# Kernel tuning notes

Hardware: AMD Instinct MI355X
Metric: run time of the kernel (lower is better)

## Reference

```python
import jax, jax.numpy as jnp
import numpy as np

B, S, H = 1, 4096, 2048
NH, HD = 16, 128  # num_heads, head_dim = H // NH


def setup_inputs() -> dict:
    key = jax.random.key(0)
    k1, k2, k3 = jax.random.split(key, 3)
    x = jax.random.normal(k1, (B, S, H), dtype=jnp.float32)
    w_qkv = jax.random.normal(k2, (3 * H, H), dtype=jnp.float32) * (1.0 / np.sqrt(H))
    w_out = jax.random.normal(k3, (H, H), dtype=jnp.float32) * (1.0 / np.sqrt(H))
    return {"x": x, "w_qkv": w_qkv, "w_out": w_out}


def reference(x, w_qkv, w_out):
    b, s, _ = x.shape
    # qkv projection: torch Linear computes x @ W^T
    qkv = jnp.einsum('bsh,oh->bso', x, w_qkv)
    qkv = qkv.reshape(b, s, 3, NH, HD).transpose(2, 0, 3, 1, 4)  # [3,B,NH,S,HD]
    q, k, v = qkv[0], qkv[1], qkv[2]
    # world_size == 1 -> single ring step == full attention with online softmax
    scores = jnp.einsum('bhqd,bhkd->bhqk', q, k) / np.sqrt(HD)
    m = jnp.max(scores, axis=-1, keepdims=True)          # running max (single step)
    p = jnp.exp(scores - m)                              # scores_exp
    out = jnp.einsum('bhqk,bhkd->bhqd', p, v)
    denom = jnp.sum(p, axis=-1, keepdims=True) + 1e-8    # running_sum + eps
    out = out / denom
    out = out.transpose(0, 2, 1, 3).reshape(b, s, H)     # [B,S,H]
    return jnp.einsum('bsh,oh->bso', out, w_out)
```

## Files before the change

kernel.cpp:

```cpp
#include <hip/hip_runtime.h>
#include <stdint.h>

typedef __attribute__((ext_vector_type(4))) float f32x4;
typedef __attribute__((ext_vector_type(16))) float f32x16;
typedef __attribute__((ext_vector_type(8))) short bf16x8;
typedef unsigned short u16;

#define MFMA(a, b, c) __builtin_amdgcn_mfma_f32_16x16x32_bf16(a, b, c, 0, 0, 0)
#define MFMA32(a, b, c) __builtin_amdgcn_mfma_f32_32x32x16_bf16(a, b, c, 0, 0, 0)
#define EXP2(x) __builtin_amdgcn_exp2f(x)
#define FENCE asm volatile("" ::: "memory")
#define BARRIER do { FENCE; __builtin_amdgcn_s_barrier(); FENCE; } while (0)

__device__ __forceinline__ u16 f2bf(float f) {
  union { float f; unsigned u; } x; x.f = f;
  unsigned r = x.u + 0x7fffu + ((x.u >> 16) & 1u);
  return (u16)(r >> 16);
}

__device__ __forceinline__ unsigned cvtpk(float lo, float hi) {
  unsigned r;
  asm("v_cvt_pk_bf16_f32 %0, %1, %2" : "=v"(r) : "v"(lo), "v"(hi));
  return r;
}

__device__ __forceinline__ void pl32swap(unsigned& a, unsigned& b) {
  asm volatile("v_permlane32_swap_b32 %0, %1" : "+v"(a), "+v"(b));
}

__device__ __forceinline__ void gload16(const void* g, void* l) {
  __builtin_amdgcn_global_load_lds(
      (const __attribute__((address_space(1))) unsigned int*)g,
      (__attribute__((address_space(3))) unsigned int*)l, 16, 0, 0);
}

__global__ void __launch_bounds__(256) cast_bf16(const float* __restrict__ in,
                                                 u16* __restrict__ out, int n4) {
  int i = blockIdx.x * 256 + threadIdx.x;
  if (i >= n4) return;
  float4 v = reinterpret_cast<const float4*>(in)[i];
  ushort4 o;
  o.x = f2bf(v.x); o.y = f2bf(v.y); o.z = f2bf(v.z); o.w = f2bf(v.w);
  reinterpret_cast<ushort4*>(out)[i] = o;
}

template <int EPI>
__global__ void __launch_bounds__(512)
gemm8(const u16* __restrict__ A, const u16* __restrict__ B,
      void* __restrict__ C0, void* __restrict__ C1, void* __restrict__ C2,
      int M, int N, int K, int MBt) {
  __shared__ alignas(16) char smb[131072];
  const int tid = threadIdx.x;
  const int w = tid >> 6, lane = tid & 63;
  const int lr = lane & 15, g = lane >> 4;
  const int wm = w >> 2, wn = w & 3;
  const int gb = (blockIdx.x & 7) * ((int)gridDim.x >> 3) + (blockIdx.x >> 3);
  const int mb = gb % MBt, nb = gb / MBt;
  const int m0 = mb * 256, n0 = nb * 256;
  const int NT = K >> 6, NIT = NT >> 1;

  const int l8 = lane >> 3, l7 = lane & 7;
  const int csb = (l7 ^ l8) * 16;
  const char* asrcb[2];
  const char* bsrcb[2];
  unsigned adst[2], bdst[2];
#pragma unroll
  for (int j = 0; j < 2; ++j) {
    int c = 2 * w + j;
    int ra = (c & 7) * 8 + ((c >> 3) << 7) + l8;
    asrcb[j] = (const char*)(A + (size_t)(m0 + ra) * K) + csb;
    adst[j] = (unsigned)(ra * 128 + l7 * 16);
    int rb = (c & 3) * 8 + ((c >> 2) << 6) + l8;
    bsrcb[j] = (const char*)(B + (size_t)(n0 + rb) * K) + csb;
    bdst[j] = (unsigned)(rb * 128 + l7 * 16);
  }
  const size_t arow64 = (size_t)64 * K * 2;
  const size_t brow32 = (size_t)32 * K * 2;

#define STG(kt, u)                                                            \
  do {                                                                        \
    if ((kt) < NT) {                                                          \
      int _d = ((kt) & 1) ? 32768 : 0;                                        \
      size_t _ko = (size_t)(kt) * 128;                                        \
      if ((u) == 0) {                                                         \
        gload16(asrcb[0] + _ko, smb + _d + adst[0]);                          \
        gload16(asrcb[1] + _ko, smb + _d + adst[1]);                          \
      } else if ((u) == 1) {                                                  \
        gload16(bsrcb[0] + _ko, smb + 65536 + _d + bdst[0]);                  \
        gload16(bsrcb[1] + _ko, smb + 65536 + _d + bdst[1]);                  \
      } else if ((u) == 2) {                                                  \
        gload16(asrcb[0] + arow64 + _ko, smb + _d + 8192 + adst[0]);          \
        gload16(asrcb[1] + arow64 + _ko, smb + _d + 8192 + adst[1]);          \
      } else {                                                                \
        gload16(bsrcb[0] + brow32 + _ko, smb + 65536 + _d + 4096 + bdst[0]);  \
        gload16(bsrcb[1] + brow32 + _ko, smb + 65536 + _d + 4096 + bdst[1]);  \
      }                                                                       \
    }                                                                         \
  } while (0)

  f32x4 acc[8][4];
#pragma unroll
  for (int x = 0; x < 8; ++x)
#pragma unroll
    for (int y = 0; y < 4; ++y) acc[x][y] = f32x4{0.f, 0.f, 0.f, 0.f};
  bf16x8 af[4][2], bf01[2][2], bf23[2][2];
  const int aoff0 = ((g) ^ (lr & 7)) << 4;
  const int aoff1 = ((4 + g) ^ (lr & 7)) << 4;
  const int arow = (wm * 128 + lr) * 128;
  const int brow = (wn * 64 + lr) * 128;

  auto LDA = [&](const char* base, int mih) {
#pragma unroll
    for (int mi = 0; mi < 4; ++mi) {
      const char* p = base + arow + (mih * 64 + mi * 16) * 128;
      af[mi][0] = *(const bf16x8*)(p + aoff0);
      af[mi][1] = *(const bf16x8*)(p + aoff1);
    }
  };
  auto LDB = [&](const char* base, bf16x8 (*bfr)[2], int nih) {
#pragma unroll
    for (int ni = 0; ni < 2; ++ni) {
      const char* p = base + brow + (nih * 32 + ni * 16) * 128;
      bfr[ni][0] = *(const bf16x8*)(p + aoff0);
      bfr[ni][1] = *(const bf16x8*)(p + aoff1);
    }
  };
  auto MM = [&](int mih, int nih, bf16x8 (*bfr)[2]) {
    __builtin_amdgcn_s_setprio(1);
#pragma unroll
    for (int mi = 0; mi < 4; ++mi)
#pragma unroll
      for (int ni = 0; ni < 2; ++ni) {
        acc[mih * 4 + mi][nih * 2 + ni] =
            MFMA(af[mi][0], bfr[ni][0], acc[mih * 4 + mi][nih * 2 + ni]);
        acc[mih * 4 + mi][nih * 2 + ni] =
            MFMA(af[mi][1], bfr[ni][1], acc[mih * 4 + mi][nih * 2 + ni]);
      }
    __builtin_amdgcn_s_setprio(0);
  };

  STG(0, 0); STG(0, 1); STG(0, 2); STG(0, 3);
  STG(1, 0); STG(1, 1); STG(1, 2);
  asm volatile("s_waitcnt vmcnt(6)" ::: "memory");
  BARRIER;

  const char* A0 = smb;
  const char* B0 = smb + 65536;
  const char* A1 = smb + 32768;
  const char* B1 = smb + 65536 + 32768;

  for (int it = 0; it < NIT; ++it) {
    const int t0 = 2 * it;
    const bool lastit = (it == NIT - 1);
    LDA(A0, 0); LDB(B0, bf01, 0); STG(t0 + 1, 3);
    BARRIER; MM(0, 0, bf01); BARRIER;
    LDB(B0, bf23, 1); STG(t0 + 2, 0);
    BARRIER; MM(0, 1, bf23); BARRIER;
    LDA(A0, 1); STG(t0 + 2, 1);
    BARRIER; MM(1, 1, bf23); BARRIER;
    STG(t0 + 2, 2);
    if (lastit) asm volatile("s_waitcnt vmcnt(0)" ::: "memory");
    else        asm volatile("s_waitcnt vmcnt(6)" ::: "memory");
    BARRIER; MM(1, 0, bf01); BARRIER;
    LDA(A1, 0); LDB(B1, bf01, 0); STG(t0 + 2, 3);
    BARRIER; MM(0, 0, bf01); BARRIER;
    LDB(B1, bf23, 1); STG(t0 + 3, 0);
    BARRIER; MM(0, 1, bf23); BARRIER;
    LDA(A1, 1); STG(t0 + 3, 1);
    BARRIER; MM(1, 1, bf23); BARRIER;
    STG(t0 + 3, 2);
    asm volatile("s_waitcnt vmcnt(6)" ::: "memory");
    BARRIER; MM(1, 0, bf01); BARRIER;
  }
#undef STG

  if (EPI == 0) {
    const float qs = 0.08838834764831845f * 1.4426950408889634f;
    u16* qo = (u16*)C0;
    u16* ko = (u16*)C1;
    u16* vo = (u16*)C2;
#pragma unroll
    for (int mi = 0; mi < 8; ++mi) {
      int s0 = m0 + wm * 128 + mi * 16 + g * 4;
#pragma unroll
      for (int ni = 0; ni < 4; ++ni) {
        int n = n0 + wn * 64 + ni * 16 + lr;
        int t = n >> 11, hh = (n >> 7) & 15, d = n & 127;
        if (t == 2) {
          ushort4 pk;
          pk.x = f2bf(acc[mi][ni][0]);
          pk.y = f2bf(acc[mi][ni][1]);
          pk.z = f2bf(acc[mi][ni][2]);
          pk.w = f2bf(acc[mi][ni][3]);
          *(ushort4*)(vo + (size_t)(hh * 128 + d) * 4096 + s0) = pk;
        } else {
          float sc = (t == 0) ? qs : 1.f;
          u16* dq = (t == 0 ? qo : ko) + (size_t)(hh * 4096 + s0) * 128 + d;
#pragma unroll
          for (int j = 0; j < 4; ++j) dq[(size_t)j * 128] = f2bf(acc[mi][ni][j] * sc);
        }
      }
    }
  } else {
    float* C = (float*)C0;
#pragma unroll
    for (int mi = 0; mi < 8; ++mi)
#pragma unroll
      for (int ni = 0; ni < 4; ++ni) {
        size_t r0 = (size_t)(m0 + wm * 128 + mi * 16 + g * 4);
        int cn = n0 + wn * 64 + ni * 16 + lr;
#pragma unroll
        for (int j = 0; j < 4; ++j) C[(r0 + j) * N + cn] = acc[mi][ni][j];
      }
  }
}

template <int EPI>
__global__ void __launch_bounds__(256, 2)
gemm_bt(const u16* __restrict__ A, const u16* __restrict__ B,
        void* __restrict__ C0, void* __restrict__ C1, void* __restrict__ C2,
        int M, int N, int K, int MB) {
  __shared__ alignas(16) u16 sm[8192];
  const int tid = threadIdx.x;
  const int w = tid >> 6, lane = tid & 63;
  const int lr = lane & 15, g = lane >> 4;
  const int gb = (blockIdx.x & 7) * ((int)gridDim.x >> 3) + (blockIdx.x >> 3);
  const int mb = gb % MB, nb = gb / MB;
  const int m0 = mb * 128, n0 = nb * 128;

  const u16* src[4];
  u16* dst[4];
#pragma unroll
  for (int i = 0; i < 4; ++i) {
    int c = w * 4 + i;
    int r = (c & 7) * 16 + (lane >> 2);
    int sb = (lane & 3) ^ ((r >> 1) & 3);
    src[i] = (c < 8) ? (A + (size_t)(m0 + r) * K + sb * 8)
                     : (B + (size_t)(n0 + r) * K + sb * 8);
    dst[i] = &sm[c * 512];
  }

  f32x4 acc[4][4];
#pragma unroll
  for (int x = 0; x < 4; ++x)
#pragma unroll
    for (int y = 0; y < 4; ++y) acc[x][y] = f32x4{0.f, 0.f, 0.f, 0.f};

  const int rowb = (w >> 1) * 64, colb = (w & 1) * 64;
  const int nk = K >> 5;
  for (int kt = 0; kt < nk; ++kt) {
#pragma unroll
    for (int i = 0; i < 4; ++i) gload16(src[i] + kt * 32, dst[i]);
    __syncthreads();
    bf16x8 af[4], bfr[4];
#pragma unroll
    for (int mi = 0; mi < 4; ++mi) {
      int r = rowb + mi * 16 + lr;
      af[mi] = *(const bf16x8*)((const char*)sm + r * 64 +
                                ((g * 16) ^ (((r >> 1) & 3) << 4)));
    }
#pragma unroll
    for (int ni = 0; ni < 4; ++ni) {
      int r = colb + ni * 16 + lr;
      bfr[ni] = *(const bf16x8*)((const char*)sm + 8192 + r * 64 +
                                 ((g * 16) ^ (((r >> 1) & 3) << 4)));
    }
#pragma unroll
    for (int mi = 0; mi < 4; ++mi)
#pragma unroll
      for (int ni = 0; ni < 4; ++ni)
        acc[mi][ni] = MFMA(af[mi], bfr[ni], acc[mi][ni]);
    __syncthreads();
  }

  float* C = (float*)C0;
#pragma unroll
  for (int mi = 0; mi < 4; ++mi)
#pragma unroll
    for (int ni = 0; ni < 4; ++ni) {
      size_t r0 = (size_t)(m0 + rowb + mi * 16 + g * 4);
      int cn = n0 + colb + ni * 16 + lr;
#pragma unroll
      for (int j = 0; j < 4; ++j) C[(r0 + j) * N + cn] = acc[mi][ni][j];
    }
}

__global__ void __launch_bounds__(512)
attn_kernel(const u16* __restrict__ qg, const u16* __restrict__ kg,
            const u16* __restrict__ vtg, u16* __restrict__ og) {
  __shared__ alignas(16) u16 sm[32768];
  const int tid = threadIdx.x;
  const int w = tid >> 6, lane = tid & 63;
  const int ql = lane & 31, hl = lane >> 5;
  const int gb = (blockIdx.x & 7) * 32 + (blockIdx.x >> 3);
  const int h = gb >> 4;
  const int qb = gb & 15;

  const u16* ssrc[4];
  u16* sdst[4];
  size_t sstep;
  if (w < 4) {
    sstep = 64 * 128;
#pragma unroll
    for (int i = 0; i < 4; ++i) {
      int c = w * 4 + i;
      int r = c * 4 + (lane >> 4);
      int sb = (lane & 15) ^ (r & 15);
      ssrc[i] = kg + (size_t)(h * 4096 + r) * 128 + sb * 8;
      sdst[i] = &sm[c * 512];
    }
  } else {
    sstep = 64;
#pragma unroll
    for (int i = 0; i < 4; ++i) {
      int c = (w - 4) * 4 + i;
      int j = c * 4 + (lane >> 4);
      int x = (lane & 15) ^ (j & 15);
      int e = x >> 3, b = x & 7;
      ssrc[i] = vtg + (size_t)(h * 128 + 2 * j + e) * 4096 + b * 8;
      sdst[i] = &sm[16384 + c * 512];
    }
  }

  const u16* qrow = qg + (size_t)(h * 4096 + qb * 256 + w * 32 + ql) * 128 + hl * 8;
  bf16x8 qf[8];
#pragma unroll
  for (int s = 0; s < 8; ++s) qf[s] = *(const bf16x8*)(qrow + s * 16);

  f32x16 of[4];
#pragma unroll
  for (int i = 0; i < 4; ++i)
#pragma unroll
    for (int r = 0; r < 16; ++r) of[i][r] = 0.f;
  float mrun = -1e30f, lsum = 0.f;
  const float thr = 6.0f;

#pragma unroll
  for (int i = 0; i < 4; ++i) gload16(ssrc[i], sdst[i]);

  const int kxor = (ql & 15) << 4;
  const int ve8 = (ql & 1) << 3, vxor = ql >> 1;
  for (int t = 0; t < 64; ++t) {
    const int cur = t & 1;
    asm volatile("s_waitcnt vmcnt(0)" ::: "memory");
    __builtin_amdgcn_s_barrier();
    FENCE;
    if (t + 1 < 64) {
      const int nb = (t + 1) & 1;
#pragma unroll
      for (int i = 0; i < 4; ++i)
        gload16(ssrc[i] + (size_t)(t + 1) * sstep, sdst[i] + nb * 8192);
    }
    const char* kbuf = (const char*)sm + cur * 16384;
    const char* vbuf = (const char*)sm + 32768 + cur * 16384;

    f32x16 st0, st1;
#pragma unroll
    for (int r = 0; r < 16; ++r) { st0[r] = 0.f; st1[r] = 0.f; }
    __builtin_amdgcn_s_setprio(1);
#pragma unroll
    for (int s = 0; s < 8; ++s) {
      int off = ((s * 2 + hl) << 4) ^ kxor;
      bf16x8 k0 = *(const bf16x8*)(kbuf + ql * 256 + off);
      bf16x8 k1 = *(const bf16x8*)(kbuf + (32 + ql) * 256 + off);
      st0 = MFMA32(k0, qf[s], st0);
      st1 = MFMA32(k1, qf[s], st1);
    }
    __builtin_amdgcn_s_setprio(0);

    float tmax = -1e30f;
#pragma unroll
    for (int r = 0; r < 16; ++r) tmax = fmaxf(tmax, fmaxf(st0[r], st1[r]));
    tmax = fmaxf(tmax, __shfl_xor(tmax, 32));
    if (!__all(tmax - mrun <= thr)) {
      float mnew = fmaxf(mrun, tmax);
      float esc = EXP2(mrun - mnew);
#pragma unroll
      for (int db = 0; db < 4; ++db)
#pragma unroll
        for (int r = 0; r < 16; ++r) of[db][r] *= esc;
      lsum *= esc;
      mrun = mnew;
    }
    float psum = 0.f;
    unsigned pk0[8], pk1[8];
#pragma unroll
    for (int i = 0; i < 8; ++i) {
      float a0 = EXP2(st0[2 * i] - mrun);
      float b0 = EXP2(st0[2 * i + 1] - mrun);
      float a1 = EXP2(st1[2 * i] - mrun);
      float b1 = EXP2(st1[2 * i + 1] - mrun);
      psum += (a0 + b0) + (a1 + b1);
      pk0[i] = cvtpk(a0, b0);
      pk1[i] = cvtpk(a1, b1);
    }
    psum += __shfl_xor(psum, 32);
    lsum += psum;

    pl32swap(pk0[0], pk0[2]); pl32swap(pk0[1], pk0[3]);
    pl32swap(pk0[4], pk0[6]); pl32swap(pk0[5], pk0[7]);
    pl32swap(pk1[0], pk1[2]); pl32swap(pk1[1], pk1[3]);
    pl32swap(pk1[4], pk1[6]); pl32swap(pk1[5], pk1[7]);
    union U { unsigned u[4]; bf16x8 v; };
    U paf[4];
#pragma unroll
    for (int i = 0; i < 4; ++i) { paf[0].u[i] = pk0[i]; paf[1].u[i] = pk0[4 + i]; }
#pragma unroll
    for (int i = 0; i < 4; ++i) { paf[2].u[i] = pk1[i]; paf[3].u[i] = pk1[4 + i]; }

    __builtin_amdgcn_s_setprio(1);
#pragma unroll
    for (int db = 0; db < 4; ++db) {
      const char* vrow = vbuf + (db * 16 + vxor) * 256;
#pragma unroll
      for (int kp = 0; kp < 4; ++kp) {
        int m = (ve8 | (kp * 2 + hl)) ^ vxor;
        bf16x8 vf = *(const bf16x8*)(vrow + m * 16);
        of[db] = MFMA32(vf, paf[kp].v, of[db]);
      }
    }
    __builtin_amdgcn_s_setprio(0);
    FENCE;
  }

  float linv = 1.f / (lsum + 1e-8f);
  size_t qrow_o = (size_t)(qb * 256 + w * 32 + ql) * 2048 + h * 128;
#pragma unroll
  for (int db = 0; db < 4; ++db)
#pragma unroll
    for (int u = 0; u < 4; ++u) {
      ushort4 pk;
      pk.x = f2bf(of[db][4 * u + 0] * linv);
      pk.y = f2bf(of[db][4 * u + 1] * linv);
      pk.z = f2bf(of[db][4 * u + 2] * linv);
      pk.w = f2bf(of[db][4 * u + 3] * linv);
      *(ushort4*)(og + qrow_o + db * 32 + 8 * u + hl * 4) = pk;
    }
}

extern "C" void kernel_launch(void* const* d_in, const int* in_sizes, int n_in,
                              void* d_out, int out_size, void* d_ws, size_t ws_size,
                              hipStream_t stream) {
  const float* x = (const float*)d_in[0];
  const float* w_qkv = (const float*)d_in[1];
  const float* w_out = (const float*)d_in[2];

  char* ws = (char*)d_ws;
  u16* xb = (u16*)(ws + 0);
  u16* wqkvb = (u16*)(ws + 16777216);
  u16* woutb = (u16*)(ws + 41943040);
  u16* qb = (u16*)(ws + 50331648);
  u16* kb = (u16*)(ws + 67108864);
  u16* vtb = (u16*)(ws + 83886080);
  u16* aob = (u16*)(ws + 100663296);

  cast_bf16<<<8192, 256, 0, stream>>>(x, xb, 2097152);
  cast_bf16<<<12288, 256, 0, stream>>>(w_qkv, wqkvb, 3145728);
  cast_bf16<<<4096, 256, 0, stream>>>(w_out, woutb, 1048576);

  gemm8<0><<<384, 512, 0, stream>>>(xb, wqkvb, qb, kb, vtb, 4096, 6144, 2048, 16);
  attn_kernel<<<256, 512, 0, stream>>>(qb, kb, vtb, aob);
  gemm_bt<1><<<32 * 16, 256, 0, stream>>>(aob, woutb, d_out, nullptr, nullptr, 4096, 2048, 2048, 32);
}
```

Before: 339.6 us.

## Split attention KV range across two wave groups with LDS merge of partials

The attention kernel now handles 128 query rows per block instead of 256, doubling the grid to 512 blocks. Each block's two groups of four waves process separate halves of the key/value sequence (split-K), each with its own smaller 32-key double-buffered tiles. At the end the two partial softmax states (max, sum, output accumulators) are exchanged through LDS and merged by the first group before writing. The aim is more blocks across the 256 CUs and less work per wave per tile. The cost is an extra LDS round trip, a merge step, and a larger LDS footprint (about 66 KB), which may limit blocks per CU.

```diff
diff --git a/kernel.cpp b/kernel.cpp
--- a/kernel.cpp
+++ b/kernel.cpp
@@ -288,41 +288,46 @@
 __global__ void __launch_bounds__(512)
 attn_kernel(const u16* __restrict__ qg, const u16* __restrict__ kg,
             const u16* __restrict__ vtg, u16* __restrict__ og) {
-  __shared__ alignas(16) u16 sm[32768];
+  __shared__ alignas(64) char smb[67584];
   const int tid = threadIdx.x;
   const int w = tid >> 6, lane = tid & 63;
   const int ql = lane & 31, hl = lane >> 5;
-  const int gb = (blockIdx.x & 7) * 32 + (blockIdx.x >> 3);
-  const int h = gb >> 4;
-  const int qb = gb & 15;
+  const int gb = (blockIdx.x & 7) * 64 + (blockIdx.x >> 3);
+  const int h = gb >> 5;
+  const int qb = gb & 31;
+  const int g2 = w >> 2;
+  const int qw = w & 3;
 
   const u16* ssrc[4];
-  u16* sdst[4];
+  unsigned sdst[4];
   size_t sstep;
-  if (w < 4) {
-    sstep = 64 * 128;
-#pragma unroll
-    for (int i = 0; i < 4; ++i) {
-      int c = w * 4 + i;
-      int r = c * 4 + (lane >> 4);
-      int sb = (lane & 15) ^ (r & 15);
-      ssrc[i] = kg + (size_t)(h * 4096 + r) * 128 + sb * 8;
-      sdst[i] = &sm[c * 512];
-    }
-  } else {
-    sstep = 64;
-#pragma unroll
-    for (int i = 0; i < 4; ++i) {
-      int c = (w - 4) * 4 + i;
-      int j = c * 4 + (lane >> 4);
-      int x = (lane & 15) ^ (j & 15);
-      int e = x >> 3, b = x & 7;
-      ssrc[i] = vtg + (size_t)(h * 128 + 2 * j + e) * 4096 + b * 8;
-      sdst[i] = &sm[16384 + c * 512];
-    }
-  }
-
-  const u16* qrow = qg + (size_t)(h * 4096 + qb * 256 + w * 32 + ql) * 128 + hl * 8;
+  {
+    const int sg = w >> 2;
+    if (!((w >> 1) & 1)) {
+      sstep = 32 * 128;
+#pragma unroll
+      for (int i = 0; i < 4; ++i) {
+        int c = (w & 1) * 4 + i;
+        int r = c * 4 + (lane >> 4);
+        int sb = (lane & 15) ^ (r & 15);
+        ssrc[i] = kg + (size_t)(h * 4096 + sg * 2048 + r) * 128 + sb * 8;
+        sdst[i] = sg * 16384 + c * 1024;
+      }
+    } else {
+      sstep = 32;
+#pragma unroll
+      for (int i = 0; i < 4; ++i) {
+        int c = (w & 1) * 4 + i;
+        int j = c * 4 + (lane >> 4);
+        int x = (lane & 15) ^ (j & 15);
+        int e = x >> 2, b = x & 3;
+        ssrc[i] = vtg + (size_t)(h * 128 + 4 * j + e) * 4096 + sg * 2048 + b * 8;
+        sdst[i] = 32768 + sg * 16384 + c * 1024;
+      }
+    }
+  }
+
+  const u16* qrow = qg + (size_t)(h * 4096 + qb * 128 + qw * 32 + ql) * 128 + hl * 8;
   bf16x8 qf[8];
 #pragma unroll
   for (int s = 0; s < 8; ++s) qf[s] = *(const bf16x8*)(qrow + s * 16);
@@ -336,10 +341,14 @@
   const float thr = 6.0f;
 
 #pragma unroll
-  for (int i = 0; i < 4; ++i) gload16(ssrc[i], sdst[i]);
+  for (int i = 0; i < 4; ++i) gload16(ssrc[i], smb + sdst[i]);
 
   const int kxor = (ql & 15) << 4;
-  const int ve8 = (ql & 1) << 3, vxor = ql >> 1;
+  const char* kbase = smb + g2 * 16384;
+  const char* vbase = smb + 32768 + g2 * 16384;
+  const int vj = ql >> 2;
+  const int vm0 = (ql & 3) << 2;
+
   for (int t = 0; t < 64; ++t) {
     const int cur = t & 1;
     asm volatile("s_waitcnt vmcnt(0)" ::: "memory");
@@ -349,28 +358,26 @@
       const int nb = (t + 1) & 1;
 #pragma unroll
       for (int i = 0; i < 4; ++i)
-        gload16(ssrc[i] + (size_t)(t + 1) * sstep, sdst[i] + nb * 8192);
-    }
-    const char* kbuf = (const char*)sm + cur * 16384;
-    const char* vbuf = (const char*)sm + 32768 + cur * 16384;
-
-    f32x16 st0, st1;
-#pragma unroll
-    for (int r = 0; r < 16; ++r) { st0[r] = 0.f; st1[r] = 0.f; }
+        gload16(ssrc[i] + (size_t)(t + 1) * sstep, smb + sdst[i] + nb * 8192);
+    }
+    const char* kbuf = kbase + cur * 8192;
+    const char* vbuf = vbase + cur * 8192;
+
+    f32x16 st0;
+#pragma unroll
+    for (int r = 0; r < 16; ++r) st0[r] = 0.f;
     __builtin_amdgcn_s_setprio(1);
 #pragma unroll
     for (int s = 0; s < 8; ++s) {
       int off = ((s * 2 + hl) << 4) ^ kxor;
       bf16x8 k0 = *(const bf16x8*)(kbuf + ql * 256 + off);
-      bf16x8 k1 = *(const bf16x8*)(kbuf + (32 + ql) * 256 + off);
       st0 = MFMA32(k0, qf[s], st0);
-      st1 = MFMA32(k1, qf[s], st1);
     }
     __builtin_amdgcn_s_setprio(0);
 
     float tmax = -1e30f;
 #pragma unroll
-    for (int r = 0; r < 16; ++r) tmax = fmaxf(tmax, fmaxf(st0[r], st1[r]));
+    for (int r = 0; r < 16; ++r) tmax = fmaxf(tmax, st0[r]);
     tmax = fmaxf(tmax, __shfl_xor(tmax, 32));
     if (!__all(tmax - mrun <= thr)) {
       float mnew = fmaxf(mrun, tmax);
@@ -383,38 +390,32 @@
       mrun = mnew;
     }
     float psum = 0.f;
-    unsigned pk0[8], pk1[8];
+    unsigned pk0[8];
 #pragma unroll
     for (int i = 0; i < 8; ++i) {
       float a0 = EXP2(st0[2 * i] - mrun);
       float b0 = EXP2(st0[2 * i + 1] - mrun);
-      float a1 = EXP2(st1[2 * i] - mrun);
-      float b1 = EXP2(st1[2 * i + 1] - mrun);
-      psum += (a0 + b0) + (a1 + b1);
+      psum += a0 + b0;
       pk0[i] = cvtpk(a0, b0);
-      pk1[i] = cvtpk(a1, b1);
     }
     psum += __shfl_xor(psum, 32);
     lsum += psum;
 
     pl32swap(pk0[0], pk0[2]); pl32swap(pk0[1], pk0[3]);
     pl32swap(pk0[4], pk0[6]); pl32swap(pk0[5], pk0[7]);
-    pl32swap(pk1[0], pk1[2]); pl32swap(pk1[1], pk1[3]);
-    pl32swap(pk1[4], pk1[6]); pl32swap(pk1[5], pk1[7]);
     union U { unsigned u[4]; bf16x8 v; };
-    U paf[4];
+    U paf[2];
 #pragma unroll
     for (int i = 0; i < 4; ++i) { paf[0].u[i] = pk0[i]; paf[1].u[i] = pk0[4 + i]; }
-#pragma unroll
-    for (int i = 0; i < 4; ++i) { paf[2].u[i] = pk1[i]; paf[3].u[i] = pk1[4 + i]; }
 
     __builtin_amdgcn_s_setprio(1);
 #pragma unroll
     for (int db = 0; db < 4; ++db) {
-      const char* vrow = vbuf + (db * 16 + vxor) * 256;
-#pragma unroll
-      for (int kp = 0; kp < 4; ++kp) {
-        int m = (ve8 | (kp * 2 + hl)) ^ vxor;
+      int j = db * 8 + vj;
+      const char* vrow = vbuf + j * 256;
+#pragma unroll
+      for (int kp = 0; kp < 2; ++kp) {
+        int m = (vm0 | (kp * 2 + hl)) ^ (j & 15);
         bf16x8 vf = *(const bf16x8*)(vrow + m * 16);
         of[db] = MFMA32(vf, paf[kp].v, of[db]);
       }
@@ -423,19 +424,40 @@
     FENCE;
   }
 
-  float linv = 1.f / (lsum + 1e-8f);
-  size_t qrow_o = (size_t)(qb * 256 + w * 32 + ql) * 2048 + h * 128;
-#pragma unroll
-  for (int db = 0; db < 4; ++db)
-#pragma unroll
-    for (int u = 0; u < 4; ++u) {
-      ushort4 pk;
-      pk.x = f2bf(of[db][4 * u + 0] * linv);
-      pk.y = f2bf(of[db][4 * u + 1] * linv);
-      pk.z = f2bf(of[db][4 * u + 2] * linv);
-      pk.w = f2bf(of[db][4 * u + 3] * linv);
-      *(ushort4*)(og + qrow_o + db * 32 + 8 * u + hl * 4) = pk;
-    }
+  __syncthreads();
+  if (w >= 4) {
+    char* base = smb + qw * 16384 + lane * 256;
+#pragma unroll
+    for (int db = 0; db < 4; ++db) *(f32x16*)(base + db * 64) = of[db];
+    float2 ml;
+    ml.x = mrun; ml.y = lsum;
+    *(float2*)(smb + 65536 + (qw * 64 + lane) * 8) = ml;
+  }
+  __syncthreads();
+  if (w < 4) {
+    const char* base = smb + qw * 16384 + lane * 256;
+    float2 ml = *(const float2*)(smb + 65536 + (qw * 64 + lane) * 8);
+    float m = fmaxf(mrun, ml.x);
+    float a0 = EXP2(mrun - m);
+    float a1 = EXP2(ml.x - m);
+    float l = lsum * a0 + ml.y * a1;
+    float linv = 1.f / (l + 1e-8f);
+    float fa0 = a0 * linv, fa1 = a1 * linv;
+    size_t qrow_o = (size_t)(qb * 128 + qw * 32 + ql) * 2048 + h * 128;
+#pragma unroll
+    for (int db = 0; db < 4; ++db) {
+      f32x16 ob = *(const f32x16*)(base + db * 64);
+#pragma unroll
+      for (int u = 0; u < 4; ++u) {
+        ushort4 pk;
+        pk.x = f2bf(of[db][4 * u + 0] * fa0 + ob[4 * u + 0] * fa1);
+        pk.y = f2bf(of[db][4 * u + 1] * fa0 + ob[4 * u + 1] * fa1);
+        pk.z = f2bf(of[db][4 * u + 2] * fa0 + ob[4 * u + 2] * fa1);
+        pk.w = f2bf(of[db][4 * u + 3] * fa0 + ob[4 * u + 3] * fa1);
+        *(ushort4*)(og + qrow_o + db * 32 + 8 * u + hl * 4) = pk;
+      }
+    }
+  }
 }
 
 extern "C" void kernel_launch(void* const* d_in, const int* in_sizes, int n_in,
@@ -459,6 +481,6 @@
   cast_bf16<<<4096, 256, 0, stream>>>(w_out, woutb, 1048576);
 
   gemm8<0><<<384, 512, 0, stream>>>(xb, wqkvb, qb, kb, vtb, 4096, 6144, 2048, 16);
-  attn_kernel<<<256, 512, 0, stream>>>(qb, kb, vtb, aob);
+  attn_kernel<<<512, 512, 0, stream>>>(qb, kb, vtb, aob);
   gemm_bt<1><<<32 * 16, 256, 0, stream>>>(aob, woutb, d_out, nullptr, nullptr, 4096, 2048, 2048, 32);
 }
```

Result: slower. 362.1 us (+6.6%).

## Widen attention KV tile to 128 keys and reuse gemm8 for output projection

Applied to the files above, without the earlier changes.

The attention kernel now processes 128 keys per iteration instead of 64. That halves the loop trip count and the barrier count, using 128KB of double-buffered LDS with a simpler swizzled V layout. The output projection switches from the small 128x128 gemm_bt kernel to the larger-tile gemm8 kernel in its fp32 epilogue mode, and gemm_bt is deleted. The trade-offs are more registers for four score accumulators, a full 128KB of LDS per attention block, and only 128 blocks for the final GEMM, which may underfill the 256 CUs.

```diff
diff --git a/kernel.cpp b/kernel.cpp
--- a/kernel.cpp
+++ b/kernel.cpp
@@ -215,80 +215,10 @@
   }
 }
 
-template <int EPI>
-__global__ void __launch_bounds__(256, 2)
-gemm_bt(const u16* __restrict__ A, const u16* __restrict__ B,
-        void* __restrict__ C0, void* __restrict__ C1, void* __restrict__ C2,
-        int M, int N, int K, int MB) {
-  __shared__ alignas(16) u16 sm[8192];
-  const int tid = threadIdx.x;
-  const int w = tid >> 6, lane = tid & 63;
-  const int lr = lane & 15, g = lane >> 4;
-  const int gb = (blockIdx.x & 7) * ((int)gridDim.x >> 3) + (blockIdx.x >> 3);
-  const int mb = gb % MB, nb = gb / MB;
-  const int m0 = mb * 128, n0 = nb * 128;
-
-  const u16* src[4];
-  u16* dst[4];
-#pragma unroll
-  for (int i = 0; i < 4; ++i) {
-    int c = w * 4 + i;
-    int r = (c & 7) * 16 + (lane >> 2);
-    int sb = (lane & 3) ^ ((r >> 1) & 3);
-    src[i] = (c < 8) ? (A + (size_t)(m0 + r) * K + sb * 8)
-                     : (B + (size_t)(n0 + r) * K + sb * 8);
-    dst[i] = &sm[c * 512];
-  }
-
-  f32x4 acc[4][4];
-#pragma unroll
-  for (int x = 0; x < 4; ++x)
-#pragma unroll
-    for (int y = 0; y < 4; ++y) acc[x][y] = f32x4{0.f, 0.f, 0.f, 0.f};
-
-  const int rowb = (w >> 1) * 64, colb = (w & 1) * 64;
-  const int nk = K >> 5;
-  for (int kt = 0; kt < nk; ++kt) {
-#pragma unroll
-    for (int i = 0; i < 4; ++i) gload16(src[i] + kt * 32, dst[i]);
-    __syncthreads();
-    bf16x8 af[4], bfr[4];
-#pragma unroll
-    for (int mi = 0; mi < 4; ++mi) {
-      int r = rowb + mi * 16 + lr;
-      af[mi] = *(const bf16x8*)((const char*)sm + r * 64 +
-                                ((g * 16) ^ (((r >> 1) & 3) << 4)));
-    }
-#pragma unroll
-    for (int ni = 0; ni < 4; ++ni) {
-      int r = colb + ni * 16 + lr;
-      bfr[ni] = *(const bf16x8*)((const char*)sm + 8192 + r * 64 +
-                                 ((g * 16) ^ (((r >> 1) & 3) << 4)));
-    }
-#pragma unroll
-    for (int mi = 0; mi < 4; ++mi)
-#pragma unroll
-      for (int ni = 0; ni < 4; ++ni)
-        acc[mi][ni] = MFMA(af[mi], bfr[ni], acc[mi][ni]);
-    __syncthreads();
-  }
-
-  float* C = (float*)C0;
-#pragma unroll
-  for (int mi = 0; mi < 4; ++mi)
-#pragma unroll
-    for (int ni = 0; ni < 4; ++ni) {
-      size_t r0 = (size_t)(m0 + rowb + mi * 16 + g * 4);
-      int cn = n0 + colb + ni * 16 + lr;
-#pragma unroll
-      for (int j = 0; j < 4; ++j) C[(r0 + j) * N + cn] = acc[mi][ni][j];
-    }
-}
-
 __global__ void __launch_bounds__(512)
 attn_kernel(const u16* __restrict__ qg, const u16* __restrict__ kg,
             const u16* __restrict__ vtg, u16* __restrict__ og) {
-  __shared__ alignas(16) u16 sm[32768];
+  __shared__ alignas(64) char smb[131072];
   const int tid = threadIdx.x;
   const int w = tid >> 6, lane = tid & 63;
   const int ql = lane & 31, hl = lane >> 5;
@@ -296,29 +226,28 @@
   const int h = gb >> 4;
   const int qb = gb & 15;
 
-  const u16* ssrc[4];
-  u16* sdst[4];
+  const u16* ssrc[8];
+  unsigned sdst[8];
   size_t sstep;
   if (w < 4) {
-    sstep = 64 * 128;
-#pragma unroll
-    for (int i = 0; i < 4; ++i) {
-      int c = w * 4 + i;
+    sstep = 128 * 128;
+#pragma unroll
+    for (int i = 0; i < 8; ++i) {
+      int c = w * 8 + i;
       int r = c * 4 + (lane >> 4);
       int sb = (lane & 15) ^ (r & 15);
       ssrc[i] = kg + (size_t)(h * 4096 + r) * 128 + sb * 8;
-      sdst[i] = &sm[c * 512];
+      sdst[i] = c * 1024;
     }
   } else {
-    sstep = 64;
-#pragma unroll
-    for (int i = 0; i < 4; ++i) {
-      int c = (w - 4) * 4 + i;
-      int j = c * 4 + (lane >> 4);
-      int x = (lane & 15) ^ (j & 15);
-      int e = x >> 3, b = x & 7;
-      ssrc[i] = vtg + (size_t)(h * 128 + 2 * j + e) * 4096 + b * 8;
-      sdst[i] = &sm[16384 + c * 512];
+    sstep = 128;
+#pragma unroll
+    for (int i = 0; i < 8; ++i) {
+      int c = (w - 4) * 8 + i;
+      int r = c * 4 + (lane >> 4);
+      int sb = (lane & 15) ^ (r & 15);
+      ssrc[i] = vtg + (size_t)(h * 128 + r) * 4096 + sb * 8;
+      sdst[i] = 65536 + c * 1024;
     }
   }
 
@@ -336,41 +265,48 @@
   const float thr = 6.0f;
 
 #pragma unroll
-  for (int i = 0; i < 4; ++i) gload16(ssrc[i], sdst[i]);
+  for (int i = 0; i < 8; ++i) gload16(ssrc[i], smb + sdst[i]);
 
   const int kxor = (ql & 15) << 4;
-  const int ve8 = (ql & 1) << 3, vxor = ql >> 1;
-  for (int t = 0; t < 64; ++t) {
+  for (int t = 0; t < 32; ++t) {
     const int cur = t & 1;
     asm volatile("s_waitcnt vmcnt(0)" ::: "memory");
     __builtin_amdgcn_s_barrier();
     FENCE;
-    if (t + 1 < 64) {
+    if (t + 1 < 32) {
       const int nb = (t + 1) & 1;
 #pragma unroll
-      for (int i = 0; i < 4; ++i)
-        gload16(ssrc[i] + (size_t)(t + 1) * sstep, sdst[i] + nb * 8192);
-    }
-    const char* kbuf = (const char*)sm + cur * 16384;
-    const char* vbuf = (const char*)sm + 32768 + cur * 16384;
-
-    f32x16 st0, st1;
-#pragma unroll
-    for (int r = 0; r < 16; ++r) { st0[r] = 0.f; st1[r] = 0.f; }
+      for (int i = 0; i < 8; ++i)
+        gload16(ssrc[i] + (size_t)(t + 1) * sstep, smb + sdst[i] + nb * 32768);
+    }
+    const char* kbuf = smb + cur * 32768;
+    const char* vbuf = smb + 65536 + cur * 32768;
+
+    f32x16 st[4];
+#pragma unroll
+    for (int kb = 0; kb < 4; ++kb)
+#pragma unroll
+      for (int r = 0; r < 16; ++r) st[kb][r] = 0.f;
     __builtin_amdgcn_s_setprio(1);
 #pragma unroll
     for (int s = 0; s < 8; ++s) {
       int off = ((s * 2 + hl) << 4) ^ kxor;
-      bf16x8 k0 = *(const bf16x8*)(kbuf + ql * 256 + off);
-      bf16x8 k1 = *(const bf16x8*)(kbuf + (32 + ql) * 256 + off);
-      st0 = MFMA32(k0, qf[s], st0);
-      st1 = MFMA32(k1, qf[s], st1);
+      bf16x8 k0 = *(const bf16x8*)(kbuf + (0 * 32 + ql) * 256 + off);
+      bf16x8 k1 = *(const bf16x8*)(kbuf + (1 * 32 + ql) * 256 + off);
+      bf16x8 k2 = *(const bf16x8*)(kbuf + (2 * 32 + ql) * 256 + off);
+      bf16x8 k3 = *(const bf16x8*)(kbuf + (3 * 32 + ql) * 256 + off);
+      st[0] = MFMA32(k0, qf[s], st[0]);
+      st[1] = MFMA32(k1, qf[s], st[1]);
+      st[2] = MFMA32(k2, qf[s], st[2]);
+      st[3] = MFMA32(k3, qf[s], st[3]);
     }
     __builtin_amdgcn_s_setprio(0);
 
     float tmax = -1e30f;
 #pragma unroll
-    for (int r = 0; r < 16; ++r) tmax = fmaxf(tmax, fmaxf(st0[r], st1[r]));
+    for (int kb = 0; kb < 4; ++kb)
+#pragma unroll
+      for (int r = 0; r < 16; ++r) tmax = fmaxf(tmax, st[kb][r]);
     tmax = fmaxf(tmax, __shfl_xor(tmax, 32));
     if (!__all(tmax - mrun <= thr)) {
       float mnew = fmaxf(mrun, tmax);
@@ -383,38 +319,43 @@
       mrun = mnew;
     }
     float psum = 0.f;
-    unsigned pk0[8], pk1[8];
-#pragma unroll
-    for (int i = 0; i < 8; ++i) {
-      float a0 = EXP2(st0[2 * i] - mrun);
-      float b0 = EXP2(st0[2 * i + 1] - mrun);
-      float a1 = EXP2(st1[2 * i] - mrun);
-      float b1 = EXP2(st1[2 * i + 1] - mrun);
-      psum += (a0 + b0) + (a1 + b1);
-      pk0[i] = cvtpk(a0, b0);
-      pk1[i] = cvtpk(a1, b1);
+    union U { unsigned u[4]; bf16x8 v; };
+    U paf[8];
+#pragma unroll
+    for (int gp = 0; gp < 2; ++gp) {
+      unsigned pk0[8], pk1[8];
+#pragma unroll
+      for (int i = 0; i < 8; ++i) {
+        float a0 = EXP2(st[2 * gp + 0][2 * i] - mrun);
+        float b0 = EXP2(st[2 * gp + 0][2 * i + 1] - mrun);
+        float a1 = EXP2(st[2 * gp + 1][2 * i] - mrun);
+        float b1 = EXP2(st[2 * gp + 1][2 * i + 1] - mrun);
+        psum += (a0 + b0) + (a1 + b1);
+        pk0[i] = cvtpk(a0, b0);
+        pk1[i] = cvtpk(a1, b1);
+      }
+      pl32swap(pk0[0], pk0[2]); pl32swap(pk0[1], pk0[3]);
+      pl32swap(pk0[4], pk0[6]); pl32swap(pk0[5], pk0[7]);
+      pl32swap(pk1[0], pk1[2]); pl32swap(pk1[1], pk1[3]);
+      pl32swap(pk1[4], pk1[6]); pl32swap(pk1[5], pk1[7]);
+#pragma unroll
+      for (int i = 0; i < 4; ++i) {
+        paf[gp * 4 + 0].u[i] = pk0[i];
+        paf[gp * 4 + 1].u[i] = pk0[4 + i];
+        paf[gp * 4 + 2].u[i] = pk1[i];
+        paf[gp * 4 + 3].u[i] = pk1[4 + i];
+      }
     }
     psum += __shfl_xor(psum, 32);
     lsum += psum;
 
-    pl32swap(pk0[0], pk0[2]); pl32swap(pk0[1], pk0[3]);
-    pl32swap(pk0[4], pk0[6]); pl32swap(pk0[5], pk0[7]);
-    pl32swap(pk1[0], pk1[2]); pl32swap(pk1[1], pk1[3]);
-    pl32swap(pk1[4], pk1[6]); pl32swap(pk1[5], pk1[7]);
-    union U { unsigned u[4]; bf16x8 v; };
-    U paf[4];
-#pragma unroll
-    for (int i = 0; i < 4; ++i) { paf[0].u[i] = pk0[i]; paf[1].u[i] = pk0[4 + i]; }
-#pragma unroll
-    for (int i = 0; i < 4; ++i) { paf[2].u[i] = pk1[i]; paf[3].u[i] = pk1[4 + i]; }
-
     __builtin_amdgcn_s_setprio(1);
 #pragma unroll
     for (int db = 0; db < 4; ++db) {
-      const char* vrow = vbuf + (db * 16 + vxor) * 256;
-#pragma unroll
-      for (int kp = 0; kp < 4; ++kp) {
-        int m = (ve8 | (kp * 2 + hl)) ^ vxor;
+      const char* vrow = vbuf + (db * 32 + ql) * 256;
+#pragma unroll
+      for (int kp = 0; kp < 8; ++kp) {
+        int m = (kp * 2 + hl) ^ (ql & 15);
         bf16x8 vf = *(const bf16x8*)(vrow + m * 16);
         of[db] = MFMA32(vf, paf[kp].v, of[db]);
       }
@@ -460,5 +401,5 @@
 
   gemm8<0><<<384, 512, 0, stream>>>(xb, wqkvb, qb, kb, vtb, 4096, 6144, 2048, 16);
   attn_kernel<<<256, 512, 0, stream>>>(qb, kb, vtb, aob);
-  gemm_bt<1><<<32 * 16, 256, 0, stream>>>(aob, woutb, d_out, nullptr, nullptr, 4096, 2048, 2048, 32);
-}
+  gemm8<1><<<128, 512, 0, stream>>>(aob, woutb, d_out, nullptr, nullptr, 4096, 2048, 2048, 16);
+}
```

New measurement: 339.1 us. About the same (-0.2%).
